# Kernel tuning notes

Hardware: AMD Instinct MI355X
Metric: run time of the kernel (lower is better)

Reference implementation:

```python
import jax, jax.numpy as jnp
import numpy as np

B_, T_, IN_, OUT_, N_ = 16, 4096, 512, 512, 512


def setup_inputs() -> dict:
    key = jax.random.key(0)
    ks = jax.random.split(key, 9)
    u = jax.random.normal(ks[0], (B_, T_, IN_), dtype=jnp.float32)
    # LRU init per original module
    rmin, rmax, max_phase = 0.9, 1.0, 6.283
    u1 = jax.random.uniform(ks[1], (N_,), dtype=jnp.float32)
    u2 = jax.random.uniform(ks[2], (N_,), dtype=jnp.float32)
    nu_log = jnp.log(-0.5 * jnp.log(u1 * (rmax + rmin) * (rmax - rmin) + rmin ** 2))
    theta_log = jnp.log(max_phase * u2)
    Lambda_mod = jnp.exp(-jnp.exp(nu_log))
    gamma_log = jnp.log(jnp.sqrt(1.0 - jnp.square(Lambda_mod)))
    B_re = jax.random.normal(ks[3], (N_, IN_), dtype=jnp.float32) / np.sqrt(2 * IN_)
    B_im = jax.random.normal(ks[4], (N_, IN_), dtype=jnp.float32) / np.sqrt(2 * IN_)
    C_re = jax.random.normal(ks[5], (OUT_, N_), dtype=jnp.float32) / np.sqrt(N_)
    C_im = jax.random.normal(ks[6], (OUT_, N_), dtype=jnp.float32) / np.sqrt(N_)
    D = jax.random.normal(ks[7], (OUT_, IN_), dtype=jnp.float32) / np.sqrt(IN_)
    return {"u": u, "nu_log": nu_log, "theta_log": theta_log, "gamma_log": gamma_log,
            "B_re": B_re, "B_im": B_im, "C_re": C_re, "C_im": C_im, "D": D}


def reference(u, nu_log, theta_log, gamma_log, B_re, B_im, C_re, C_im, D):
    # Lambda: diagonal complex transition, |Lambda| = exp(-exp(nu_log)), angle = exp(theta_log)
    mod = jnp.exp(-jnp.exp(nu_log))             # [N]
    theta = jnp.exp(theta_log)
    Lam = jax.lax.complex(mod * jnp.cos(theta), mod * jnp.sin(theta))  # [N] complex64
    gammas = jnp.exp(gamma_log)                  # [N]
    Bc = jax.lax.complex(B_re, B_im) * gammas[:, None]                 # [N, IN]
    Cc = jax.lax.complex(C_re, C_im)                                   # [OUT, N]

    # input projection: Bu[b,t,n] = sum_i Bc[n,i] * u[b,t,i]
    Bu = jnp.einsum('bti,ni->btn', u.astype(Bc.dtype), Bc)             # [B,T,N] complex

    # diagonal linear recurrence x_t = Lam * x_{t-1} + Bu_t, state starts at 0
    a = jnp.broadcast_to(Lam, Bu.shape)

    def combine(e1, e2):
        a1, b1 = e1
        a2, b2 = e2
        return a1 * a2, a2 * b1 + b2

    _, x = jax.lax.associative_scan(combine, (a, Bu), axis=1)          # x: [B,T,N]

    y = 2.0 * jnp.einsum('btn,on->bto', x, Cc).real + jnp.einsum('bti,oi->bto', u, D)
    return y
```

## Files before the change

### kernel.cpp

```cpp
#include <hip/hip_runtime.h>
#include <hip/hip_bf16.h>
#include <cstdint>
#include <cstddef>


using short8 = __attribute__((ext_vector_type(8))) short;
using f32x4 = __attribute__((ext_vector_type(4))) float;

#define BDIM 16
#define TDIM 4096
#define MTOT (BDIM * TDIM)
#define CHUNK 64
#define NCHUNK (TDIM / CHUNK)

__device__ __forceinline__ unsigned short f2bf(float f) {
    unsigned u = __float_as_uint(f);
    u = u + 0x7FFFu + ((u >> 16) & 1u);
    return (unsigned short)(u >> 16);
}
__device__ __forceinline__ float bflo(unsigned w) { return __uint_as_float(w << 16); }
__device__ __forceinline__ float bfhi(unsigned w) { return __uint_as_float(w & 0xFFFF0000u); }

__device__ __forceinline__ size_t perm_off(int row, int kt, int kp, int rowbytes) {
    int kk = kp >> 5, km = kp & 31;
    int half = km >> 4;
    int g = (km & 15) >> 2, j = km & 3;
    int cc = (kk << 2) | g;
    int c = cc ^ (row & 7);
    return (size_t)row * rowbytes + kt * 128 + (c << 4) + half * 8 + j * 2;
}

__device__ __forceinline__ void gload_lds16(const void* g, void* l) {
    __builtin_amdgcn_global_load_lds((const __attribute__((address_space(1))) void*)g,
                                     (__attribute__((address_space(3))) void*)l, 16, 0, 0);
}

__global__ void prep_w1(const float* __restrict__ B_re, const float* __restrict__ B_im,
                        const float* __restrict__ gamma_log, char* __restrict__ W1) {
    int i = blockIdx.x * 256 + threadIdx.x;
    int r = blockIdx.y;
    int n = r >> 1;
    float gmm = expf(gamma_log[n]);
    float v = (r & 1) ? B_im[n * 512 + i] * gmm : B_re[n * 512 + i] * gmm;
    *(unsigned short*)(W1 + perm_off(r, i >> 6, i & 63, 1024)) = f2bf(v);
}

__global__ void prep_w2(const float* __restrict__ C_re, const float* __restrict__ C_im,
                        const float* __restrict__ D, char* __restrict__ W2) {
    int k = blockIdx.x * 256 + threadIdx.x;
    int o = blockIdx.y;
    float v;
    if (k < 1024) {
        int n = k >> 1;
        v = (k & 1) ? -2.0f * C_im[o * 512 + n] : 2.0f * C_re[o * 512 + n];
    } else {
        v = D[o * 512 + (k - 1024)];
    }
    *(unsigned short*)(W2 + perm_off(o, k >> 6, k & 63, 3072)) = f2bf(v);
}

__global__ void convert_u(const float4* __restrict__ u4, char* __restrict__ Apack) {
    size_t idx = (size_t)blockIdx.x * 256 + threadIdx.x;
    float4 v = u4[idx];
    int row = (int)(idx >> 7);
    int c4 = (int)(idx & 127);
    int kg = 1024 + c4 * 4;
    unsigned lo = (unsigned)f2bf(v.x) | ((unsigned)f2bf(v.y) << 16);
    unsigned hi = (unsigned)f2bf(v.z) | ((unsigned)f2bf(v.w) << 16);
    size_t off = perm_off(row, kg >> 6, kg & 63, 3072);
    *reinterpret_cast<uint2*>(Apack + off) = make_uint2(lo, hi);
}

#define ASM_VMCNT8 asm volatile("s_waitcnt vmcnt(8)" ::: "memory")
#define ASM_VMCNT0 asm volatile("s_waitcnt vmcnt(0)" ::: "memory")
#define ASM_LGKM0  asm volatile("s_waitcnt lgkmcnt(0)" ::: "memory")

template <int OUT_MODE, int NBN>
__global__ __launch_bounds__(512, 2) void gemm_nt(const char* __restrict__ A, int ldab,
                                                  const char* __restrict__ Bm, int ldbb,
                                                  void* __restrict__ Cout, int ktiles,
                                                  float2* __restrict__ carry,
                                                  const float* __restrict__ nu_log,
                                                  const float* __restrict__ theta_log) {
    __shared__ __align__(16) char lds[131072];
    const int tid = threadIdx.x;
    const int lane = tid & 63, w = tid >> 6;
    const int bid = blockIdx.x;
    const int cpx = gridDim.x >> 3;
    const int swz = (bid & 7) * cpx + (bid >> 3);
    const int bm = swz / NBN, bn = swz % NBN;
    const int wm = (w >> 2) * 128, wn = (w & 3) * 64;
    const int ml = lane & 15, g = lane >> 4;

    const char* Agr = A + (size_t)(bm * 256 + w * 32 + (lane >> 3)) * ldab + (lane & 7) * 16;
    const char* Bgr = Bm + (size_t)(bn * 256 + w * 32 + (lane & 63 ? (lane >> 3) : 0)) * ldbb + (lane & 7) * 16;
    const char* Bgr2 = Bm + (size_t)(bn * 256 + w * 32 + (lane >> 3)) * ldbb + (lane & 7) * 16;

#define STAGE(q, kt_) do {                                                            \
        _Pragma("unroll")                                                             \
        for (int p = 0; p < 4; ++p) {                                                 \
            gload_lds16(Agr + (size_t)(p * 8) * ldab + (size_t)(kt_) * 128,           \
                        lds + (q) * 65536 + w * 4096 + p * 1024);                     \
            gload_lds16(Bgr2 + (size_t)(p * 8) * ldbb + (size_t)(kt_) * 128,          \
                        lds + (q) * 65536 + 32768 + w * 4096 + p * 1024);             \
        }                                                                             \
    } while (0)

    f32x4 acc[8][4] = {};

    STAGE(0, 0);
    STAGE(1, 1);

    for (int kt = 0; kt < ktiles; ++kt) {
        const int cur = kt & 1;
        if (kt + 2 <= ktiles) { ASM_VMCNT8; } else { ASM_VMCNT0; }
        __builtin_amdgcn_s_barrier();
        __builtin_amdgcn_sched_barrier(0);
        const char* As = lds + cur * 65536;
        const char* Bs = lds + cur * 65536 + 32768;
#pragma unroll
        for (int kk = 0; kk < 2; ++kk) {
            short8 af[8], bfr[4];
#pragma unroll
            for (int mt = 0; mt < 8; ++mt) {
                int r = wm + mt * 16 + ml;
                af[mt] = *reinterpret_cast<const short8*>(
                    As + r * 128 + ((((kk << 2) | g) ^ (r & 7)) << 4));
            }
#pragma unroll
            for (int nt = 0; nt < 4; ++nt) {
                int r = wn + nt * 16 + ml;
                bfr[nt] = *reinterpret_cast<const short8*>(
                    Bs + r * 128 + ((((kk << 2) | g) ^ (r & 7)) << 4));
            }
            __builtin_amdgcn_s_setprio(1);
#pragma unroll
            for (int mt = 0; mt < 8; ++mt)
#pragma unroll
                for (int nt = 0; nt < 4; ++nt)
                    acc[mt][nt] = __builtin_amdgcn_mfma_f32_16x16x32_bf16(af[mt], bfr[nt], acc[mt][nt], 0, 0, 0);
            __builtin_amdgcn_s_setprio(0);
        }
        ASM_LGKM0;
        __builtin_amdgcn_s_barrier();
        if (kt + 2 < ktiles) STAGE(cur, kt + 2);
    }

    if (OUT_MODE == 0) {
        float* O = (float*)Cout;
#pragma unroll
        for (int mt = 0; mt < 8; ++mt)
#pragma unroll
            for (int nt = 0; nt < 4; ++nt)
#pragma unroll
                for (int r_ = 0; r_ < 4; ++r_) {
                    int grow = bm * 256 + wm + mt * 16 + g * 4 + r_;
                    int gcol = bn * 256 + wn + nt * 16 + ml;
                    O[(size_t)grow * 512 + gcol] = acc[mt][nt][r_];
                }
    } else {
        unsigned short* BuOut = (unsigned short*)Cout;
#pragma unroll
        for (int mt = 0; mt < 8; ++mt)
#pragma unroll
            for (int nt = 0; nt < 4; ++nt)
#pragma unroll
                for (int r_ = 0; r_ < 4; ++r_) {
                    int lrow = wm + mt * 16 + g * 4 + r_;
                    int lcol = wn + nt * 16 + ml;
                    unsigned short hv = f2bf(acc[mt][nt][r_]);
                    *(unsigned short*)(lds + lrow * 512 + lcol * 2) = hv;
                    BuOut[(size_t)(bm * 256 + lrow) * 1024 + bn * 256 + lcol] = hv;
                }
        ASM_LGKM0;
        __builtin_amdgcn_s_barrier();
        __builtin_amdgcn_sched_barrier(0);
        int n_local = tid & 127, c_local = tid >> 7;
        int nglob = bn * 128 + n_local;
        float mod = expf(-expf(nu_log[nglob]));
        float th = expf(theta_log[nglob]);
        float s, co;
        sincosf(th, &s, &co);
        float Lre = mod * co, Lim = mod * s;
        const char* base = lds + (c_local * 64) * 512 + n_local * 4;
        float xr = 0.f, xi = 0.f;
#pragma unroll 8
        for (int t = 0; t < 64; ++t) {
            unsigned wv = *reinterpret_cast<const unsigned*>(base + t * 512);
            float nr = fmaf(Lre, xr, fmaf(-Lim, xi, bflo(wv)));
            float ni = fmaf(Lre, xi, fmaf(Lim, xr, bfhi(wv)));
            xr = nr; xi = ni;
        }
        int b = (bm * 256) >> 12;
        int cglob = (((bm * 256) & 4095) >> 6) + c_local;
        carry[(size_t)(b * NCHUNK + cglob) * 512 + nglob] = make_float2(xr, xi);
    }
#undef STAGE
}

__global__ void scan_prefix(const float2* __restrict__ carry, const float* __restrict__ nu_log,
                            const float* __restrict__ theta_log, float2* __restrict__ prefix) {
    int q = blockIdx.x * 256 + threadIdx.x;
    int n = q & 511, b = q >> 9;
    float e = expf(nu_log[n]);
    float modL = expf(-(float)CHUNK * e);
    float th = expf(theta_log[n]);
    double ang = fmod((double)CHUNK * (double)th, 6.283185307179586);
    float s, co;
    sincosf((float)ang, &s, &co);
    float Lre = modL * co, Lim = modL * s;
    float pr = 0.f, pi = 0.f;
    for (int c = 0; c < NCHUNK; ++c) {
        size_t idx = (size_t)(b * NCHUNK + c) * 512 + n;
        prefix[idx] = make_float2(pr, pi);
        float2 ev = carry[idx];
        float nr = fmaf(Lre, pr, fmaf(-Lim, pi, ev.x));
        float ni = fmaf(Lre, pi, fmaf(Lim, pr, ev.y));
        pr = nr; pi = ni;
    }
}

__global__ void scan_apply(const unsigned* __restrict__ Bu, const float* __restrict__ nu_log,
                           const float* __restrict__ theta_log, const float2* __restrict__ prefix,
                           char* __restrict__ Apack) {
    int q = blockIdx.x * 256 + threadIdx.x;
    int n = q & 511, c = (q >> 9) & 63, b = q >> 15;
    float mod = expf(-expf(nu_log[n]));
    float th = expf(theta_log[n]);
    float s, co;
    sincosf(th, &s, &co);
    float Lre = mod * co, Lim = mod * s;
    const unsigned* p = Bu + ((size_t)(b * TDIM + c * CHUNK)) * 512 + n;
    float2 pv = prefix[(size_t)(b * NCHUNK + c) * 512 + n];
    float xr = pv.x, xi = pv.y;
    int kp = (2 * n) & 63;
    int kk = kp >> 5, km = kp & 31;
    int half = km >> 4, gg = (km & 15) >> 2, j = km & 3;
    int cc = (kk << 2) | gg;
    int partial = (n >> 5) * 128 + half * 8 + j * 2;
    int row0 = b * TDIM + c * CHUNK;
#pragma unroll 8
    for (int t = 0; t < CHUNK; ++t) {
        unsigned wv = p[(size_t)t * 512];
        float nr = fmaf(Lre, xr, fmaf(-Lim, xi, bflo(wv)));
        float ni = fmaf(Lre, xi, fmaf(Lim, xr, bfhi(wv)));
        xr = nr; xi = ni;
        int row = row0 + t;
        size_t off = (size_t)row * 3072 + ((cc ^ (row & 7)) << 4) + partial;
        *reinterpret_cast<unsigned*>(Apack + off) =
            (unsigned)f2bf(xr) | ((unsigned)f2bf(xi) << 16);
    }
}

extern "C" void kernel_launch(void* const* d_in, const int* in_sizes, int n_in,
                              void* d_out, int out_size, void* d_ws, size_t ws_size,
                              hipStream_t stream) {
    const float* u         = (const float*)d_in[0];
    const float* nu_log    = (const float*)d_in[1];
    const float* theta_log = (const float*)d_in[2];
    const float* gamma_log = (const float*)d_in[3];
    const float* B_re      = (const float*)d_in[4];
    const float* B_im      = (const float*)d_in[5];
    const float* C_re      = (const float*)d_in[6];
    const float* C_im      = (const float*)d_in[7];
    const float* D         = (const float*)d_in[8];

    char* ws = (char*)d_ws;
    char* Apack = ws;
    size_t off = (size_t)MTOT * 3072;
    char* W1 = ws + off; off += 1024 * 1024;
    char* W2 = ws + off; off += 512 * 3072;
    float2* carry  = (float2*)(ws + off); off += (size_t)BDIM * NCHUNK * 512 * 8;
    float2* prefix = (float2*)(ws + off); off += (size_t)BDIM * NCHUNK * 512 * 8;

    unsigned short* Bu = (unsigned short*)d_out;

    prep_w1<<<dim3(2, 1024), 256, 0, stream>>>(B_re, B_im, gamma_log, W1);
    prep_w2<<<dim3(6, 512), 256, 0, stream>>>(C_re, C_im, D, W2);
    convert_u<<<32768, 256, 0, stream>>>((const float4*)u, Apack);
    gemm_nt<1, 4><<<1024, 512, 0, stream>>>(Apack + 16 * 128, 3072, W1, 1024,
                                            (void*)Bu, 8, carry, nu_log, theta_log);
    scan_prefix<<<32, 256, 0, stream>>>(carry, nu_log, theta_log, prefix);
    scan_apply<<<2048, 256, 0, stream>>>((const unsigned*)Bu, nu_log, theta_log, prefix, Apack);
    gemm_nt<0, 2><<<512, 512, 0, stream>>>(Apack, 3072, W2, 3072, d_out, 24,
                                           nullptr, nullptr, nullptr);
}
```

Measured before the change: 320.2 us.

## Restructure GEMM main loop into interleaved quadrant MFMA and staged prefetch schedule

The GEMM K-loop is rewritten from a two-tile-ahead prefetch with a bulk LDS read and 32-MFMA block into a ping-pong schedule. Each iteration splits into four MFMA quadrants, and each LDS fragment read and one slice of the next tile's global-to-LDS load is interleaved between them. The goal is to overlap global loads, LDS reads and matrix ops more finely and cut the vmcnt stall at the loop top. In exchange it adds many more barriers per iteration and only one tile of lookahead, which could expose global latency.

After: 309.5 us. 1.03x faster.

```diff
diff --git a/kernel.cpp b/kernel.cpp
--- a/kernel.cpp
+++ b/kernel.cpp
@@ -71,9 +71,11 @@
     *reinterpret_cast<uint2*>(Apack + off) = make_uint2(lo, hi);
 }
 
-#define ASM_VMCNT8 asm volatile("s_waitcnt vmcnt(8)" ::: "memory")
+#define ASM_VMCNT2 asm volatile("s_waitcnt vmcnt(2)" ::: "memory")
 #define ASM_VMCNT0 asm volatile("s_waitcnt vmcnt(0)" ::: "memory")
 #define ASM_LGKM0  asm volatile("s_waitcnt lgkmcnt(0)" ::: "memory")
+#define SCHED0     __builtin_amdgcn_sched_barrier(0)
+#define BARRIER    __builtin_amdgcn_s_barrier()
 
 template <int OUT_MODE, int NBN>
 __global__ __launch_bounds__(512, 2) void gemm_nt(const char* __restrict__ A, int ldab,
@@ -93,57 +95,79 @@
     const int ml = lane & 15, g = lane >> 4;
 
     const char* Agr = A + (size_t)(bm * 256 + w * 32 + (lane >> 3)) * ldab + (lane & 7) * 16;
-    const char* Bgr = Bm + (size_t)(bn * 256 + w * 32 + (lane & 63 ? (lane >> 3) : 0)) * ldbb + (lane & 7) * 16;
-    const char* Bgr2 = Bm + (size_t)(bn * 256 + w * 32 + (lane >> 3)) * ldbb + (lane & 7) * 16;
-
-#define STAGE(q, kt_) do {                                                            \
-        _Pragma("unroll")                                                             \
-        for (int p = 0; p < 4; ++p) {                                                 \
-            gload_lds16(Agr + (size_t)(p * 8) * ldab + (size_t)(kt_) * 128,           \
-                        lds + (q) * 65536 + w * 4096 + p * 1024);                     \
-            gload_lds16(Bgr2 + (size_t)(p * 8) * ldbb + (size_t)(kt_) * 128,          \
-                        lds + (q) * 65536 + 32768 + w * 4096 + p * 1024);             \
-        }                                                                             \
+    const char* Bgr = Bm + (size_t)(bn * 256 + w * 32 + (lane >> 3)) * ldbb + (lane & 7) * 16;
+
+#define STAGE_P(q, kt_, p) do {                                                       \
+        gload_lds16(Agr + (size_t)((p) * 8) * ldab + (size_t)(kt_) * 128,             \
+                    lds + (q) * 65536 + w * 4096 + (p) * 1024);                       \
+        gload_lds16(Bgr + (size_t)((p) * 8) * ldbb + (size_t)(kt_) * 128,             \
+                    lds + (q) * 65536 + 32768 + w * 4096 + (p) * 1024);               \
     } while (0)
 
+#define RD_A(arr, mtb, mt, kk) do {                                                   \
+        int r_ = wm + ((mtb) + (mt)) * 16 + ml;                                       \
+        arr[mt][kk] = *reinterpret_cast<const short8*>(                               \
+            As + r_ * 128 + (((((kk) << 2) | g) ^ (r_ & 7)) << 4));                   \
+    } while (0)
+
+#define RD_B(nt, kk) do {                                                             \
+        int r_ = wn + (nt) * 16 + ml;                                                 \
+        bfv[nt][kk] = *reinterpret_cast<const short8*>(                               \
+            Bs + r_ * 128 + (((((kk) << 2) | g) ^ (r_ & 7)) << 4));                   \
+    } while (0)
+
+#define MFMA_Q(arr, mtb, ntb)                                                         \
+    _Pragma("unroll")                                                                 \
+    for (int mt = 0; mt < 4; ++mt)                                                    \
+    _Pragma("unroll")                                                                 \
+    for (int nt = 0; nt < 2; ++nt)                                                    \
+    _Pragma("unroll")                                                                 \
+    for (int kk = 0; kk < 2; ++kk)                                                    \
+        acc[(mtb) + mt][(ntb) + nt] = __builtin_amdgcn_mfma_f32_16x16x32_bf16(        \
+            arr[mt][kk], bfv[(ntb) + nt][kk], acc[(mtb) + mt][(ntb) + nt], 0, 0, 0)
+
     f32x4 acc[8][4] = {};
-
-    STAGE(0, 0);
-    STAGE(1, 1);
+    short8 afA[4][2], afB[4][2], bfv[4][2];
+
+#pragma unroll
+    for (int p = 0; p < 4; ++p) STAGE_P(0, 0, p);
 
     for (int kt = 0; kt < ktiles; ++kt) {
-        const int cur = kt & 1;
-        if (kt + 2 <= ktiles) { ASM_VMCNT8; } else { ASM_VMCNT0; }
-        __builtin_amdgcn_s_barrier();
-        __builtin_amdgcn_sched_barrier(0);
+        const int cur = kt & 1, nq = cur ^ 1;
         const char* As = lds + cur * 65536;
-        const char* Bs = lds + cur * 65536 + 32768;
-#pragma unroll
-        for (int kk = 0; kk < 2; ++kk) {
-            short8 af[8], bfr[4];
-#pragma unroll
-            for (int mt = 0; mt < 8; ++mt) {
-                int r = wm + mt * 16 + ml;
-                af[mt] = *reinterpret_cast<const short8*>(
-                    As + r * 128 + ((((kk << 2) | g) ^ (r & 7)) << 4));
-            }
-#pragma unroll
-            for (int nt = 0; nt < 4; ++nt) {
-                int r = wn + nt * 16 + ml;
-                bfr[nt] = *reinterpret_cast<const short8*>(
-                    Bs + r * 128 + ((((kk << 2) | g) ^ (r & 7)) << 4));
-            }
-            __builtin_amdgcn_s_setprio(1);
-#pragma unroll
-            for (int mt = 0; mt < 8; ++mt)
-#pragma unroll
-                for (int nt = 0; nt < 4; ++nt)
-                    acc[mt][nt] = __builtin_amdgcn_mfma_f32_16x16x32_bf16(af[mt], bfr[nt], acc[mt][nt], 0, 0, 0);
-            __builtin_amdgcn_s_setprio(0);
-        }
-        ASM_LGKM0;
-        __builtin_amdgcn_s_barrier();
-        if (kt + 2 < ktiles) STAGE(cur, kt + 2);
+        const char* Bs = As + 32768;
+        const bool pre = (kt + 1 < ktiles);
+        if (pre) { STAGE_P(nq, kt + 1, 0); ASM_VMCNT2; } else { ASM_VMCNT0; }
+        SCHED0;
+        BARRIER;
+#pragma unroll
+        for (int mt = 0; mt < 4; ++mt) { RD_A(afA, 0, mt, 0); RD_A(afA, 0, mt, 1); }
+        RD_B(0, 0); RD_B(0, 1); RD_B(1, 0); RD_B(1, 1);
+        if (pre) STAGE_P(nq, kt + 1, 1);
+        SCHED0; BARRIER; ASM_LGKM0; SCHED0;
+        __builtin_amdgcn_s_setprio(1);
+        MFMA_Q(afA, 0, 0);
+        __builtin_amdgcn_s_setprio(0);
+        BARRIER;
+        RD_B(2, 0); RD_B(2, 1); RD_B(3, 0); RD_B(3, 1);
+        if (pre) STAGE_P(nq, kt + 1, 2);
+        SCHED0; BARRIER; ASM_LGKM0; SCHED0;
+        __builtin_amdgcn_s_setprio(1);
+        MFMA_Q(afA, 0, 2);
+        __builtin_amdgcn_s_setprio(0);
+        BARRIER;
+#pragma unroll
+        for (int mt = 0; mt < 4; ++mt) { RD_A(afB, 4, mt, 0); RD_A(afB, 4, mt, 1); }
+        if (pre) STAGE_P(nq, kt + 1, 3);
+        SCHED0; BARRIER; ASM_LGKM0; SCHED0;
+        __builtin_amdgcn_s_setprio(1);
+        MFMA_Q(afB, 4, 0);
+        __builtin_amdgcn_s_setprio(0);
+        BARRIER;
+        SCHED0;
+        __builtin_amdgcn_s_setprio(1);
+        MFMA_Q(afB, 4, 2);
+        __builtin_amdgcn_s_setprio(0);
     }
 
     if (OUT_MODE == 0) {
@@ -173,8 +197,8 @@
                     BuOut[(size_t)(bm * 256 + lrow) * 1024 + bn * 256 + lcol] = hv;
                 }
         ASM_LGKM0;
-        __builtin_amdgcn_s_barrier();
-        __builtin_amdgcn_sched_barrier(0);
+        BARRIER;
+        SCHED0;
         int n_local = tid & 127, c_local = tid >> 7;
         int nglob = bn * 128 + n_local;
         float mod = expf(-expf(nu_log[nglob]));
@@ -195,7 +219,10 @@
         int cglob = (((bm * 256) & 4095) >> 6) + c_local;
         carry[(size_t)(b * NCHUNK + cglob) * 512 + nglob] = make_float2(xr, xi);
     }
-#undef STAGE
+#undef STAGE_P
+#undef RD_A
+#undef RD_B
+#undef MFMA_Q
 }
 
 __global__ void scan_prefix(const float2* __restrict__ carry, const float* __restrict__ nu_log,
```

## Restructure GEMM main loop into 8-phase interleaved load/MFMA schedule

Applied to the files above, without the earlier changes.

Replaces the double-buffered per-K-tile loop with a two-tile unrolled schedule that splits each tile into four quadrant MFMA phases. Global-to-LDS stages for half-tiles of A and B are interleaved between the phases, and LDS fragment reads are staged per quadrant with barriers. The aim is finer-grained overlap of global loads, LDS reads and MFMA work, in the style of hipBLASLt-like ping-pong kernels. It adds many more barriers and assumes ktiles is even, with tight vmcnt accounting.

Result: faster. 294.7 us (-8.0%).

```diff
diff --git a/kernel.cpp b/kernel.cpp
--- a/kernel.cpp
+++ b/kernel.cpp
@@ -71,9 +71,13 @@
     *reinterpret_cast<uint2*>(Apack + off) = make_uint2(lo, hi);
 }
 
-#define ASM_VMCNT8 asm volatile("s_waitcnt vmcnt(8)" ::: "memory")
+#define ASM_VMCNT4 asm volatile("s_waitcnt vmcnt(4)" ::: "memory")
 #define ASM_VMCNT0 asm volatile("s_waitcnt vmcnt(0)" ::: "memory")
 #define ASM_LGKM0  asm volatile("s_waitcnt lgkmcnt(0)" ::: "memory")
+#define SCHED0     __builtin_amdgcn_sched_barrier(0)
+#define BARRIER    __builtin_amdgcn_s_barrier()
+#define PRIO1      __builtin_amdgcn_s_setprio(1)
+#define PRIO0      __builtin_amdgcn_s_setprio(0)
 
 template <int OUT_MODE, int NBN>
 __global__ __launch_bounds__(512, 2) void gemm_nt(const char* __restrict__ A, int ldab,
@@ -92,58 +96,102 @@
     const int wm = (w >> 2) * 128, wn = (w & 3) * 64;
     const int ml = lane & 15, g = lane >> 4;
 
-    const char* Agr = A + (size_t)(bm * 256 + w * 32 + (lane >> 3)) * ldab + (lane & 7) * 16;
-    const char* Bgr = Bm + (size_t)(bn * 256 + w * 32 + (lane & 63 ? (lane >> 3) : 0)) * ldbb + (lane & 7) * 16;
-    const char* Bgr2 = Bm + (size_t)(bn * 256 + w * 32 + (lane >> 3)) * ldbb + (lane & 7) * 16;
-
-#define STAGE(q, kt_) do {                                                            \
-        _Pragma("unroll")                                                             \
-        for (int p = 0; p < 4; ++p) {                                                 \
-            gload_lds16(Agr + (size_t)(p * 8) * ldab + (size_t)(kt_) * 128,           \
-                        lds + (q) * 65536 + w * 4096 + p * 1024);                     \
-            gload_lds16(Bgr2 + (size_t)(p * 8) * ldbb + (size_t)(kt_) * 128,          \
-                        lds + (q) * 65536 + 32768 + w * 4096 + p * 1024);             \
-        }                                                                             \
+    const char* AgrL = A + (size_t)(bm * 256 + w * 16 + (lane >> 3)) * ldab + (lane & 7) * 16;
+    const char* BgrL = Bm + (size_t)(bn * 256 + w * 16 + (lane >> 3)) * ldbb + (lane & 7) * 16;
+
+#define STG_A(h, kt_, q) do {                                                         \
+        const char* s_ = AgrL + (size_t)((h) * 128) * ldab + (size_t)(kt_) * 128;     \
+        char* d_ = lds + (q) * 65536 + (h) * 16384 + w * 2048;                        \
+        gload_lds16(s_, d_);                                                          \
+        gload_lds16(s_ + (size_t)8 * ldab, d_ + 1024);                                \
     } while (0)
+#define STG_B(h, kt_, q) do {                                                         \
+        const char* s_ = BgrL + (size_t)((h) * 128) * ldbb + (size_t)(kt_) * 128;     \
+        char* d_ = lds + (q) * 65536 + 32768 + (h) * 16384 + w * 2048;                \
+        gload_lds16(s_, d_);                                                          \
+        gload_lds16(s_ + (size_t)8 * ldbb, d_ + 1024);                                \
+    } while (0)
+
+#define RD_A_(mh, Abase) do {                                                         \
+        _Pragma("unroll") for (int mt = 0; mt < 4; ++mt)                              \
+        _Pragma("unroll") for (int kk = 0; kk < 2; ++kk) {                            \
+            int r_ = wm + (mh) * 64 + mt * 16 + ml;                                   \
+            int hf_ = r_ >> 7, rl_ = r_ & 127;                                        \
+            afr[mt][kk] = *reinterpret_cast<const short8*>(                           \
+                (Abase) + hf_ * 16384 + rl_ * 128 + ((((kk << 2) | g) ^ (rl_ & 7)) << 4)); \
+        } } while (0)
+#define RD_B_(nh, Bbase) do {                                                         \
+        _Pragma("unroll") for (int nt = 0; nt < 2; ++nt)                              \
+        _Pragma("unroll") for (int kk = 0; kk < 2; ++kk) {                            \
+            int c_ = wn + (nh) * 32 + nt * 16 + ml;                                   \
+            int hf_ = c_ >> 7, cl_ = c_ & 127;                                        \
+            bfr[nh][nt][kk] = *reinterpret_cast<const short8*>(                       \
+                (Bbase) + hf_ * 16384 + cl_ * 128 + ((((kk << 2) | g) ^ (cl_ & 7)) << 4)); \
+        } } while (0)
+
+#define MFMA16(mh, nh)                                                                \
+    _Pragma("unroll") for (int kk = 0; kk < 2; ++kk)                                  \
+    _Pragma("unroll") for (int mt = 0; mt < 4; ++mt)                                  \
+    _Pragma("unroll") for (int nt = 0; nt < 2; ++nt)                                  \
+        acc[(mh) * 4 + mt][(nh) * 2 + nt] = __builtin_amdgcn_mfma_f32_16x16x32_bf16(  \
+            afr[mt][kk], bfr[nh][nt][kk], acc[(mh) * 4 + mt][(nh) * 2 + nt], 0, 0, 0)
 
     f32x4 acc[8][4] = {};
-
-    STAGE(0, 0);
-    STAGE(1, 1);
-
-    for (int kt = 0; kt < ktiles; ++kt) {
-        const int cur = kt & 1;
-        if (kt + 2 <= ktiles) { ASM_VMCNT8; } else { ASM_VMCNT0; }
-        __builtin_amdgcn_s_barrier();
-        __builtin_amdgcn_sched_barrier(0);
-        const char* As = lds + cur * 65536;
-        const char* Bs = lds + cur * 65536 + 32768;
-#pragma unroll
-        for (int kk = 0; kk < 2; ++kk) {
-            short8 af[8], bfr[4];
-#pragma unroll
-            for (int mt = 0; mt < 8; ++mt) {
-                int r = wm + mt * 16 + ml;
-                af[mt] = *reinterpret_cast<const short8*>(
-                    As + r * 128 + ((((kk << 2) | g) ^ (r & 7)) << 4));
-            }
-#pragma unroll
-            for (int nt = 0; nt < 4; ++nt) {
-                int r = wn + nt * 16 + ml;
-                bfr[nt] = *reinterpret_cast<const short8*>(
-                    Bs + r * 128 + ((((kk << 2) | g) ^ (r & 7)) << 4));
-            }
-            __builtin_amdgcn_s_setprio(1);
-#pragma unroll
-            for (int mt = 0; mt < 8; ++mt)
-#pragma unroll
-                for (int nt = 0; nt < 4; ++nt)
-                    acc[mt][nt] = __builtin_amdgcn_mfma_f32_16x16x32_bf16(af[mt], bfr[nt], acc[mt][nt], 0, 0, 0);
-            __builtin_amdgcn_s_setprio(0);
-        }
-        ASM_LGKM0;
-        __builtin_amdgcn_s_barrier();
-        if (kt + 2 < ktiles) STAGE(cur, kt + 2);
+    short8 afr[4][2];
+    short8 bfr[2][2][2];
+
+    const char* A0b = lds;
+    const char* B0b = lds + 32768;
+    const char* A1b = lds + 65536;
+    const char* B1b = lds + 98304;
+
+    STG_A(0, 0, 0); STG_A(1, 0, 0); STG_B(0, 0, 0); STG_B(1, 0, 0);
+    STG_B(0, 1, 1); STG_B(1, 1, 1);
+    ASM_VMCNT4;
+    BARRIER;
+
+    const int NT = ktiles >> 1;
+    for (int it = 0; it < NT; ++it) {
+        const int t1i = 2 * it + 1, t2i = 2 * it + 2, t3i = 2 * it + 3;
+        const bool more = (t2i < ktiles);
+        RD_A_(0, A0b); RD_B_(0, B0b);
+        STG_A(0, t1i, 1);
+        BARRIER; ASM_LGKM0; SCHED0;
+        PRIO1; MFMA16(0, 0); PRIO0;
+        BARRIER;
+        RD_B_(1, B0b);
+        STG_A(1, t1i, 1);
+        BARRIER; ASM_LGKM0; SCHED0;
+        PRIO1; MFMA16(0, 1); PRIO0;
+        BARRIER;
+        RD_A_(1, A0b);
+        if (more) STG_B(0, t2i, 0);
+        BARRIER; ASM_LGKM0; SCHED0;
+        PRIO1; MFMA16(1, 0); PRIO0;
+        BARRIER;
+        if (more) STG_B(1, t2i, 0);
+        PRIO1; MFMA16(1, 1); PRIO0;
+        if (more) { ASM_VMCNT4; } else { ASM_VMCNT0; }
+        BARRIER;
+        RD_A_(0, A1b); RD_B_(0, B1b);
+        if (more) STG_A(0, t2i, 0);
+        BARRIER; ASM_LGKM0; SCHED0;
+        PRIO1; MFMA16(0, 0); PRIO0;
+        BARRIER;
+        RD_B_(1, B1b);
+        if (more) STG_A(1, t2i, 0);
+        BARRIER; ASM_LGKM0; SCHED0;
+        PRIO1; MFMA16(0, 1); PRIO0;
+        BARRIER;
+        RD_A_(1, A1b);
+        if (more) STG_B(0, t3i, 1);
+        BARRIER; ASM_LGKM0; SCHED0;
+        PRIO1; MFMA16(1, 0); PRIO0;
+        BARRIER;
+        if (more) STG_B(1, t3i, 1);
+        PRIO1; MFMA16(1, 1); PRIO0;
+        if (more) { ASM_VMCNT4; }
+        BARRIER;
     }
 
     if (OUT_MODE == 0) {
@@ -173,8 +221,8 @@
                     BuOut[(size_t)(bm * 256 + lrow) * 1024 + bn * 256 + lcol] = hv;
                 }
         ASM_LGKM0;
-        __builtin_amdgcn_s_barrier();
-        __builtin_amdgcn_sched_barrier(0);
+        BARRIER;
+        SCHED0;
         int n_local = tid & 127, c_local = tid >> 7;
         int nglob = bn * 128 + n_local;
         float mod = expf(-expf(nu_log[nglob]));
@@ -195,7 +243,11 @@
         int cglob = (((bm * 256) & 4095) >> 6) + c_local;
         carry[(size_t)(b * NCHUNK + cglob) * 512 + nglob] = make_float2(xr, xi);
     }
-#undef STAGE
+#undef STG_A
+#undef STG_B
+#undef RD_A_
+#undef RD_B_
+#undef MFMA16
 }
 
 __global__ void scan_prefix(const float2* __restrict__ carry, const float* __restrict__ nu_log,
```
